# Performance work log

Measured on AMD Instinct MI355X. Metric: run time of the kernel, lower is better.

The kernel has to match this reference:

```python
import jax, jax.numpy as jnp
import numpy as np

NUM_HEADS = 16


def setup_inputs() -> dict:
    key = jax.random.key(0)
    ks = jax.random.split(key, 7)
    B, N, C, P = 8, 1024, 1024, 64
    H, hd = NUM_HEADS, C // NUM_HEADS
    return {
        "x": jax.random.normal(ks[0], (B, N, C), jnp.float32),
        "prompt": jax.random.normal(ks[1], (B, 2, P, H, hd), jnp.float32),
        "alpha": jax.random.uniform(ks[2], (1,), jnp.float32),
        "half_alpha": jax.random.uniform(ks[3], (1,), jnp.float32),
        "Wqkv": jax.random.normal(ks[4], (3 * C, C), jnp.float32) * 0.02,
        "Wproj": jax.random.normal(ks[5], (C, C), jnp.float32) * 0.02,
        "bproj": jnp.zeros((C,), jnp.float32),
    }


def reference(x, prompt, alpha, half_alpha, Wqkv, Wproj, bproj):
    B, N, C = x.shape
    H = NUM_HEADS
    hd = C // H
    scale = hd ** -0.5
    a = alpha[0]
    ha = half_alpha[0]
    # QKV projection (no bias): [B,N,3C] -> [3,B,H,N,hd]
    qkv = (x @ Wqkv.T).reshape(B, N, 3, H, hd).transpose(2, 0, 3, 1, 4)
    q, k, v = qkv[0], qkv[1], qkv[2]
    # prompt [B,2,P,H,hd] -> [2,B,H,P,hd]
    pr = prompt.transpose(1, 0, 3, 2, 4)
    key_prefix, value_prefix = pr[0], pr[1]
    # prefix concat with elementwise scaling
    k = jnp.concatenate([key_prefix, k * ha], axis=2) * a  # [B,H,P+N,hd]
    v = jnp.concatenate([value_prefix, v * ha], axis=2) * a
    attn = jax.nn.softmax(jnp.einsum('bhqd,bhkd->bhqk', q, k) * scale, axis=-1)
    out = jnp.einsum('bhqk,bhkd->bhqd', attn, v)  # [B,H,N,hd]
    out = out.transpose(0, 2, 1, 3).reshape(B, N, C)
    return out @ Wproj.T + bproj
```

## Files before the change

kernel.cpp:

```cpp
#include <hip/hip_runtime.h>

typedef float f32x4 __attribute__((ext_vector_type(4)));
typedef short bf16x8 __attribute__((ext_vector_type(8)));

#define NB 8
#define NH 16
#define NSEQ 1024
#define NP 64
#define NKV 1088
#define NC 1024
#define NHD 64
#define BHSZ 69632

__device__ __forceinline__ unsigned short f2bf(float f) {
  unsigned int u = __builtin_bit_cast(unsigned int, f);
  u += 0x7fffu + ((u >> 16) & 1u);
  return (unsigned short)(u >> 16);
}

__device__ __forceinline__ f32x4 mfma16(bf16x8 a, bf16x8 b, f32x4 c) {
  return __builtin_amdgcn_mfma_f32_16x16x32_bf16(a, b, c, 0, 0, 0);
}

__device__ __forceinline__ size_t fa_elem(int r, int k) {
  return (size_t)(r >> 7) * 131072 + (size_t)(k >> 6) * 8192 + ((r >> 6) & 1) * 4096 +
         ((k >> 5) & 1) * 2048 + ((r >> 4) & 3) * 512 + (((k >> 3) & 3) * 16 + (r & 15)) * 8 +
         (k & 7);
}

__device__ __forceinline__ void fragpack_chunk(const float* __restrict__ src,
                                               unsigned short* __restrict__ dst, int c) {
  const int lane = c & 63, m = (c >> 6) & 3, kk = (c >> 8) & 1, wr = (c >> 9) & 1,
            t = (c >> 10) & 15, panel = c >> 14;
  const int row = panel * 128 + wr * 64 + m * 16 + (lane & 15);
  const int k = t * 64 + kk * 32 + (lane >> 4) * 8;
  const float* s = src + (size_t)row * 1024 + k;
  const float4 v0 = *(const float4*)s;
  const float4 v1 = *(const float4*)(s + 4);
  ushort4 o0, o1;
  o0.x = f2bf(v0.x); o0.y = f2bf(v0.y); o0.z = f2bf(v0.z); o0.w = f2bf(v0.w);
  o1.x = f2bf(v1.x); o1.y = f2bf(v1.y); o1.z = f2bf(v1.z); o1.w = f2bf(v1.w);
  *(ushort4*)(dst + (size_t)c * 8) = o0;
  *(ushort4*)(dst + (size_t)c * 8 + 4) = o1;
}

__global__ void pack_fused(const float* __restrict__ x, const float* __restrict__ wq,
                           const float* __restrict__ wp, const float* __restrict__ prompt,
                           unsigned short* __restrict__ xd, unsigned short* __restrict__ wqd,
                           unsigned short* __restrict__ wpd, unsigned short* __restrict__ Kf,
                           unsigned short* __restrict__ Vf, const float* __restrict__ alpha) {
  int gid = blockIdx.x * 256 + threadIdx.x;
  if (gid < 1048576) {
    fragpack_chunk(x, xd, gid);
  } else if (gid < 1441792) {
    fragpack_chunk(wq, wqd, gid - 1048576);
  } else if (gid < 1572864) {
    fragpack_chunk(wp, wpd, gid - 1441792);
  } else {
    int i = gid - 1572864;
    float a = alpha[0];
    int d4 = i & 15, p = (i >> 4) & 63, h = (i >> 10) & 15, b = i >> 14;
    const int bh = b * 16 + h;
    const int d0 = d4 * 4;
    const float4 kv4 = *(const float4*)(prompt + ((((size_t)(b * 2 + 0) * NP + p) * NH + h) * NHD + d0));
    {
      const int mk = p >> 4, lrk = p & 15, kk = d0 >> 5, lg = (d0 >> 3) & 3, e0 = d0 & 7;
      unsigned short* kd = Kf + (size_t)bh * BHSZ + ((mk * 2 + kk) * 4 + lg) * 128 + lrk * 8 + e0;
      kd[0] = f2bf(kv4.x * a); kd[1] = f2bf(kv4.y * a);
      kd[2] = f2bf(kv4.z * a); kd[3] = f2bf(kv4.w * a);
    }
    const float4 vv4 = *(const float4*)(prompt + ((((size_t)(b * 2 + 1) * NP + p) * NH + h) * NHD + d0));
    {
      const int df = d0 >> 4, kk = p >> 5, lg = (p >> 3) & 3, e = p & 7;
      unsigned short* vd = Vf + (size_t)bh * BHSZ + ((df * 2 + kk) * 4 + lg) * 128 + e;
      vd[((d0 + 0) & 15) * 8] = f2bf(vv4.x * a);
      vd[((d0 + 1) & 15) * 8] = f2bf(vv4.y * a);
      vd[((d0 + 2) & 15) * 8] = f2bf(vv4.z * a);
      vd[((d0 + 3) & 15) * 8] = f2bf(vv4.w * a);
    }
  }
}

template <int MODE>
__global__ __launch_bounds__(256, 2)
void gemm_direct(const unsigned short* __restrict__ Af, const unsigned short* __restrict__ Bf,
                 unsigned short* __restrict__ Qg, unsigned short* __restrict__ Kf,
                 unsigned short* __restrict__ Vf,
                 const float* __restrict__ alphap, const float* __restrict__ halfp,
                 float* __restrict__ Cout, const float* __restrict__ bias) {
  const int tid = threadIdx.x, lane = tid & 63, wv = tid >> 6;
  const int wr = wv >> 1, wc = wv & 1;
  const int lg = lane >> 4, lr = lane & 15;
  const int bx = blockIdx.x, by = blockIdx.y;

  const unsigned short* Ab = Af + (size_t)bx * 131072 + wr * 4096 + lane * 8;
  const unsigned short* Bb = Bf + (size_t)by * 131072 + wc * 4096 + lane * 8;

  f32x4 acc[4][4] = {};
  bf16x8 aC[2][4], bC[2][4], aN[2][4], bN[2][4];

#define LOADA(dst, t)                                                          \
  _Pragma("unroll") for (int kk = 0; kk < 2; ++kk)                             \
  _Pragma("unroll") for (int m = 0; m < 4; ++m)                                \
      dst[kk][m] = *(const bf16x8*)(Ab + (size_t)(t) * 8192 + kk * 2048 + m * 512)
#define LOADB(dst, t)                                                          \
  _Pragma("unroll") for (int kk = 0; kk < 2; ++kk)                             \
  _Pragma("unroll") for (int n = 0; n < 4; ++n)                                \
      dst[kk][n] = *(const bf16x8*)(Bb + (size_t)(t) * 8192 + kk * 2048 + n * 512)

  LOADA(aC, 0);
  LOADB(bC, 0);
#pragma unroll
  for (int t = 0; t < 16; ++t) {
    if (t < 15) { LOADA(aN, t + 1); LOADB(bN, t + 1); }
    __builtin_amdgcn_sched_barrier(0);
    __builtin_amdgcn_s_setprio(1);
#pragma unroll
    for (int kk = 0; kk < 2; ++kk)
#pragma unroll
      for (int m = 0; m < 4; ++m)
#pragma unroll
        for (int n = 0; n < 4; ++n)
          acc[m][n] = mfma16(aC[kk][m], bC[kk][n], acc[m][n]);
    __builtin_amdgcn_s_setprio(0);
#pragma unroll
    for (int kk = 0; kk < 2; ++kk)
#pragma unroll
      for (int i = 0; i < 4; ++i) { aC[kk][i] = aN[kk][i]; bC[kk][i] = bN[kk][i]; }
  }
#undef LOADA
#undef LOADB

  if constexpr (MODE == 0) {
    const int slot = (by * 128) >> 10;
    const int csIn = (by * 128) & 1023;
    const float sc = (slot == 0) ? 0.18033688011112042f : (alphap[0] * halfp[0]);
#pragma unroll
    for (int m = 0; m < 4; ++m) {
      const int grow0 = bx * 128 + wr * 64 + m * 16 + lg * 4;
#pragma unroll
      for (int n = 0; n < 4; ++n) {
        const int gcol = csIn + wc * 64 + n * 16 + lr;
        const int h = gcol >> 6, d = gcol & 63;
#pragma unroll
        for (int j = 0; j < 4; ++j) {
          const int grow = grow0 + j;
          const int b = grow >> 10, nn = grow & 1023;
          const int bh = b * 16 + h;
          const unsigned short u = f2bf(acc[m][n][j] * sc);
          if (slot == 0) {
            Qg[((size_t)bh * NSEQ + nn) * NHD + d] = u;
          } else if (slot == 1) {
            const int kv = NP + nn;
            const int t = kv >> 6, mk = (kv >> 4) & 3, lrk = kv & 15;
            const int kkk = d >> 5, lgk = (d >> 3) & 3, e = d & 7;
            Kf[(size_t)bh * BHSZ + (size_t)((t * 4 + mk) * 2 + kkk) * 512 + (lgk * 16 + lrk) * 8 + e] = u;
          } else {
            const int kv = NP + nn;
            const int t = kv >> 6, kkv = (kv >> 5) & 1, lgv = (kv >> 3) & 3, e = kv & 7;
            const int df = d >> 4, lrv = d & 15;
            Vf[(size_t)bh * BHSZ + (size_t)((t * 4 + df) * 2 + kkv) * 512 + (lgv * 16 + lrv) * 8 + e] = u;
          }
        }
      }
    }
  } else {
#pragma unroll
    for (int m = 0; m < 4; ++m) {
      const int grow0 = bx * 128 + wr * 64 + m * 16 + lg * 4;
#pragma unroll
      for (int n = 0; n < 4; ++n) {
        const int gcol = by * 128 + wc * 64 + n * 16 + lr;
        const float bb = bias[gcol];
#pragma unroll
        for (int j = 0; j < 4; ++j)
          Cout[(size_t)(grow0 + j) * NC + gcol] = acc[m][n][j] + bb;
      }
    }
  }
}

__global__ __launch_bounds__(256, 3)
void attn_fwd(const unsigned short* __restrict__ Qg, const unsigned short* __restrict__ Kf,
              const unsigned short* __restrict__ Vf, unsigned short* __restrict__ Oat) {
  __shared__ __align__(16) unsigned short Plds[4 * 32 * 64];
  const int tid = threadIdx.x, lane = tid & 63, wv = tid >> 6;
  const int bh = blockIdx.x & 127;
  const int q0 = (blockIdx.x >> 7) * 128;
  const int lg = lane >> 4, lr = lane & 15;

  bf16x8 bq[2][2];
#pragma unroll
  for (int nq = 0; nq < 2; ++nq)
#pragma unroll
    for (int kk = 0; kk < 2; ++kk)
      bq[nq][kk] = *(const bf16x8*)(Qg + ((size_t)bh * NSEQ + q0 + wv * 32 + nq * 16 + lr) * NHD + kk * 32 + lg * 8);

  f32x4 oac[2][4] = {};
  float mrun[2] = {-1e30f, -1e30f};
  float lrun[2] = {0.f, 0.f};

  const unsigned short* Kb = Kf + (size_t)bh * BHSZ + lane * 8;
  const unsigned short* Vb = Vf + (size_t)bh * BHSZ + lane * 8;
  unsigned short* Pw = Plds + wv * 2048;

  for (int t = 0; t < 17; ++t) {
    bf16x8 ak[4][2];
#pragma unroll
    for (int mk = 0; mk < 4; ++mk)
#pragma unroll
      for (int kk = 0; kk < 2; ++kk)
        ak[mk][kk] = *(const bf16x8*)(Kb + (size_t)((t * 4 + mk) * 2 + kk) * 512);

    f32x4 sa[4][2] = {};
    __builtin_amdgcn_s_setprio(1);
#pragma unroll
    for (int kk = 0; kk < 2; ++kk)
#pragma unroll
      for (int mk = 0; mk < 4; ++mk)
#pragma unroll
        for (int nq = 0; nq < 2; ++nq)
          sa[mk][nq] = mfma16(ak[mk][kk], bq[nq][kk], sa[mk][nq]);
    __builtin_amdgcn_s_setprio(0);

    bf16x8 bv[4][2];
#pragma unroll
    for (int df = 0; df < 4; ++df)
#pragma unroll
      for (int kk = 0; kk < 2; ++kk)
        bv[df][kk] = *(const bf16x8*)(Vb + (size_t)((t * 4 + df) * 2 + kk) * 512);

    float tmx[2];
#pragma unroll
    for (int nq = 0; nq < 2; ++nq) {
      f32x4 m4 = sa[0][nq];
#pragma unroll
      for (int mk = 1; mk < 4; ++mk)
#pragma unroll
        for (int j = 0; j < 4; ++j) m4[j] = fmaxf(m4[j], sa[mk][nq][j]);
      float tm = fmaxf(fmaxf(m4[0], m4[1]), fmaxf(m4[2], m4[3]));
      tm = fmaxf(tm, __shfl_xor(tm, 16));
      tm = fmaxf(tm, __shfl_xor(tm, 32));
      tmx[nq] = tm;
    }
    const bool upd = !__all((tmx[0] <= mrun[0] + 8.f) && (tmx[1] <= mrun[1] + 8.f));
    if (upd) {
      const float nm0 = fmaxf(mrun[0], tmx[0]);
      const float nm1 = fmaxf(mrun[1], tmx[1]);
      const float e0 = __builtin_amdgcn_exp2f(mrun[0] - nm0);
      const float e1 = __builtin_amdgcn_exp2f(mrun[1] - nm1);
      mrun[0] = nm0; mrun[1] = nm1;
      lrun[0] *= e0; lrun[1] *= e1;
#pragma unroll
      for (int m = 0; m < 2; ++m)
#pragma unroll
        for (int j = 0; j < 4; ++j) {
          const float fe = __shfl(m ? e1 : e0, lg * 4 + j, 16);
#pragma unroll
          for (int df = 0; df < 4; ++df) oac[m][df][j] *= fe;
        }
    }
#pragma unroll
    for (int nq = 0; nq < 2; ++nq) {
#pragma unroll
      for (int mk = 0; mk < 4; ++mk)
#pragma unroll
        for (int j = 0; j < 4; ++j)
          sa[mk][nq][j] = __builtin_amdgcn_exp2f(sa[mk][nq][j] - mrun[nq]);
      f32x4 s4 = sa[0][nq];
#pragma unroll
      for (int mk = 1; mk < 4; ++mk)
#pragma unroll
        for (int j = 0; j < 4; ++j) s4[j] += sa[mk][nq][j];
      float s = (s4[0] + s4[1]) + (s4[2] + s4[3]);
      s += __shfl_xor(s, 16);
      s += __shfl_xor(s, 32);
      lrun[nq] += s;
      const int q = nq * 16 + lr;
#pragma unroll
      for (int mk = 0; mk < 4; ++mk) {
        const int c = mk * 2 + (lg >> 1);
        uint2 uu;
        uu.x = (unsigned)f2bf(sa[mk][nq][0]) | ((unsigned)f2bf(sa[mk][nq][1]) << 16);
        uu.y = (unsigned)f2bf(sa[mk][nq][2]) | ((unsigned)f2bf(sa[mk][nq][3]) << 16);
        *(uint2*)(Pw + q * 64 + ((c ^ (q & 7)) << 3) + (lg & 1) * 4) = uu;
      }
    }

    __builtin_amdgcn_s_setprio(1);
#pragma unroll
    for (int kk = 0; kk < 2; ++kk) {
      bf16x8 ap[2];
#pragma unroll
      for (int m = 0; m < 2; ++m) {
        const int q = m * 16 + lr;
        const int pos = (kk * 4 + lg) ^ (q & 7);
        ap[m] = *(const bf16x8*)(Pw + q * 64 + pos * 8);
      }
#pragma unroll
      for (int m = 0; m < 2; ++m)
#pragma unroll
        for (int df = 0; df < 4; ++df)
          oac[m][df] = mfma16(ap[m], bv[df][kk], oac[m][df]);
    }
    __builtin_amdgcn_s_setprio(0);
  }

  const int bidx = bh >> 4, h = bh & 15;
  const float l0 = 1.f / lrun[0], l1 = 1.f / lrun[1];
#pragma unroll
  for (int m = 0; m < 2; ++m) {
#pragma unroll
    for (int j = 0; j < 4; ++j) {
      const float fi = __shfl(m ? l1 : l0, lg * 4 + j, 16);
      const int grow = bidx * NSEQ + q0 + wv * 32 + m * 16 + lg * 4 + j;
#pragma unroll
      for (int df = 0; df < 4; ++df) {
        const int col = h * 64 + df * 16 + lr;
        Oat[fa_elem(grow, col)] = f2bf(oac[m][df][j] * fi);
      }
    }
  }
}

extern "C" void kernel_launch(void* const* d_in, const int* in_sizes, int n_in,
                              void* d_out, int out_size, void* d_ws, size_t ws_size,
                              hipStream_t stream) {
  const float* x      = (const float*)d_in[0];
  const float* prompt = (const float*)d_in[1];
  const float* alpha  = (const float*)d_in[2];
  const float* halfa  = (const float*)d_in[3];
  const float* Wqkv   = (const float*)d_in[4];
  const float* Wproj  = (const float*)d_in[5];
  const float* bproj  = (const float*)d_in[6];
  float* out = (float*)d_out;

  unsigned short* ws    = (unsigned short*)d_ws;
  unsigned short* x_bf  = ws;
  unsigned short* w_bf  = x_bf + (size_t)8192 * 1024;
  unsigned short* wp_bf = w_bf + (size_t)3072 * 1024;
  unsigned short* Qg    = wp_bf + (size_t)1024 * 1024;
  unsigned short* Kf    = Qg + (size_t)NB * NH * NSEQ * NHD;
  unsigned short* Vf    = Kf + (size_t)128 * BHSZ;
  unsigned short* Oat   = Vf + (size_t)128 * BHSZ;

  pack_fused<<<6656, 256, 0, stream>>>(x, Wqkv, Wproj, prompt, x_bf, w_bf, wp_bf,
                                       Kf, Vf, alpha);

  gemm_direct<0><<<dim3(64, 24), 256, 0, stream>>>(x_bf, w_bf, Qg, Kf, Vf, alpha, halfa,
                                                   nullptr, nullptr);
  attn_fwd<<<1024, 256, 0, stream>>>(Qg, Kf, Vf, Oat);
  gemm_direct<1><<<dim3(64, 8), 256, 0, stream>>>(Oat, wp_bf, nullptr, nullptr, nullptr,
                                                  nullptr, nullptr, out, bproj);
}
```

Measured before the change: 165.3 us.

## Use inline-asm global loads with explicit vmcnt waits for two-deep prefetch

Replaces compiler-generated register-prefetch loads in the direct GEMM main loop with inline-assembly global_load_dwordx4 using SGPR base plus VGPR offset and immediate offsets. Two k-tiles are kept in flight in even/odd register buffers, with manual s_waitcnt vmcnt(16) so the MFMAs on one tile overlap the loads of the next two. This removes the register copies between buffers and is meant to hide global memory latency better. It depends on the asm volatile loads being counted correctly against vmcnt and on the compiler not reordering around them, and the extra in-flight buffer raises register pressure under launch bounds (256,2).

```diff
diff --git a/kernel.cpp b/kernel.cpp
--- a/kernel.cpp
+++ b/kernel.cpp
@@ -93,43 +93,67 @@
   const int lg = lane >> 4, lr = lane & 15;
   const int bx = blockIdx.x, by = blockIdx.y;
 
-  const unsigned short* Ab = Af + (size_t)bx * 131072 + wr * 4096 + lane * 8;
-  const unsigned short* Bb = Bf + (size_t)by * 131072 + wc * 4096 + lane * 8;
+  unsigned int vA0 = (unsigned)(bx * 131072 + wr * 4096 + lane * 8) * 2;
+  unsigned int vA1 = vA0 + 4096;
+  unsigned int vB0 = (unsigned)(by * 131072 + wc * 4096 + lane * 8) * 2;
+  unsigned int vB1 = vB0 + 4096;
 
   f32x4 acc[4][4] = {};
-  bf16x8 aC[2][4], bC[2][4], aN[2][4], bN[2][4];
-
-#define LOADA(dst, t)                                                          \
-  _Pragma("unroll") for (int kk = 0; kk < 2; ++kk)                             \
-  _Pragma("unroll") for (int m = 0; m < 4; ++m)                                \
-      dst[kk][m] = *(const bf16x8*)(Ab + (size_t)(t) * 8192 + kk * 2048 + m * 512)
-#define LOADB(dst, t)                                                          \
-  _Pragma("unroll") for (int kk = 0; kk < 2; ++kk)                             \
-  _Pragma("unroll") for (int n = 0; n < 4; ++n)                                \
-      dst[kk][n] = *(const bf16x8*)(Bb + (size_t)(t) * 8192 + kk * 2048 + n * 512)
-
-  LOADA(aC, 0);
-  LOADB(bC, 0);
+  bf16x8 aE[2][4], bE[2][4], aO[2][4], bO[2][4];
+
+#define GLD(dst, voff, base, imm)                                              \
+  asm volatile("global_load_dwordx4 %0, %1, %2 offset:" #imm                   \
+               : "=v"(dst) : "v"(voff), "s"(base))
+
+#define ISSUE_T(aX, bX)                                                        \
+  do {                                                                         \
+    GLD(aX[0][0], vA0, Af, 0);                                                 \
+    GLD(aX[0][1], vA0, Af, 1024);                                              \
+    GLD(aX[0][2], vA0, Af, 2048);                                              \
+    GLD(aX[0][3], vA0, Af, 3072);                                              \
+    GLD(aX[1][0], vA1, Af, 0);                                                 \
+    GLD(aX[1][1], vA1, Af, 1024);                                              \
+    GLD(aX[1][2], vA1, Af, 2048);                                              \
+    GLD(aX[1][3], vA1, Af, 3072);                                              \
+    GLD(bX[0][0], vB0, Bf, 0);                                                 \
+    GLD(bX[0][1], vB0, Bf, 1024);                                              \
+    GLD(bX[0][2], vB0, Bf, 2048);                                              \
+    GLD(bX[0][3], vB0, Bf, 3072);                                              \
+    GLD(bX[1][0], vB1, Bf, 0);                                                 \
+    GLD(bX[1][1], vB1, Bf, 1024);                                              \
+    GLD(bX[1][2], vB1, Bf, 2048);                                              \
+    GLD(bX[1][3], vB1, Bf, 3072);                                              \
+    vA0 += 16384; vA1 += 16384; vB0 += 16384; vB1 += 16384;                    \
+  } while (0)
+
+#define MFMA_T(aX, bX)                                                         \
+  do {                                                                         \
+    __builtin_amdgcn_s_setprio(1);                                             \
+    _Pragma("unroll") for (int kk = 0; kk < 2; ++kk)                           \
+    _Pragma("unroll") for (int m = 0; m < 4; ++m)                              \
+    _Pragma("unroll") for (int n = 0; n < 4; ++n)                              \
+        acc[m][n] = mfma16(aX[kk][m], bX[kk][n], acc[m][n]);                   \
+    __builtin_amdgcn_s_setprio(0);                                             \
+  } while (0)
+
+  ISSUE_T(aE, bE);
+  ISSUE_T(aO, bO);
 #pragma unroll
   for (int t = 0; t < 16; ++t) {
-    if (t < 15) { LOADA(aN, t + 1); LOADB(bN, t + 1); }
+    if (t < 15) asm volatile("s_waitcnt vmcnt(16)" ::: "memory");
+    else        asm volatile("s_waitcnt vmcnt(0)" ::: "memory");
     __builtin_amdgcn_sched_barrier(0);
-    __builtin_amdgcn_s_setprio(1);
-#pragma unroll
-    for (int kk = 0; kk < 2; ++kk)
-#pragma unroll
-      for (int m = 0; m < 4; ++m)
-#pragma unroll
-        for (int n = 0; n < 4; ++n)
-          acc[m][n] = mfma16(aC[kk][m], bC[kk][n], acc[m][n]);
-    __builtin_amdgcn_s_setprio(0);
-#pragma unroll
-    for (int kk = 0; kk < 2; ++kk)
-#pragma unroll
-      for (int i = 0; i < 4; ++i) { aC[kk][i] = aN[kk][i]; bC[kk][i] = bN[kk][i]; }
-  }
-#undef LOADA
-#undef LOADB
+    if ((t & 1) == 0) {
+      MFMA_T(aE, bE);
+      if (t + 2 < 16) ISSUE_T(aE, bE);
+    } else {
+      MFMA_T(aO, bO);
+      if (t + 2 < 16) ISSUE_T(aO, bO);
+    }
+  }
+#undef GLD
+#undef ISSUE_T
+#undef MFMA_T
 
   if constexpr (MODE == 0) {
     const int slot = (by * 128) >> 10;
```

Result: no change. 165.5 us (+0.1%).

## Split GEMM tiles across eight waves with half-tile double buffering

Applied to the files above, without the earlier changes.

The direct-from-global GEMM now runs 512 threads per block, each wave owning a 64x32 sub-tile instead of 64x64. This halves per-wave accumulator and fragment registers. The k-loop is restructured into 32 half-steps with two alternating register buffers, so loads for step s+2 are issued right after the MFMAs of step s. The aim is higher occupancy and better latency hiding, at the cost of each wave reloading its A fragments, which doubles A global/L2 traffic per block.

```diff
diff --git a/kernel.cpp b/kernel.cpp
--- a/kernel.cpp
+++ b/kernel.cpp
@@ -82,54 +82,55 @@
 }
 
 template <int MODE>
-__global__ __launch_bounds__(256, 2)
+__global__ __launch_bounds__(512, 4)
 void gemm_direct(const unsigned short* __restrict__ Af, const unsigned short* __restrict__ Bf,
                  unsigned short* __restrict__ Qg, unsigned short* __restrict__ Kf,
                  unsigned short* __restrict__ Vf,
                  const float* __restrict__ alphap, const float* __restrict__ halfp,
                  float* __restrict__ Cout, const float* __restrict__ bias) {
   const int tid = threadIdx.x, lane = tid & 63, wv = tid >> 6;
-  const int wr = wv >> 1, wc = wv & 1;
+  const int wm = wv >> 2, wn = wv & 3;
   const int lg = lane >> 4, lr = lane & 15;
   const int bx = blockIdx.x, by = blockIdx.y;
 
-  const unsigned short* Ab = Af + (size_t)bx * 131072 + wr * 4096 + lane * 8;
-  const unsigned short* Bb = Bf + (size_t)by * 131072 + wc * 4096 + lane * 8;
-
-  f32x4 acc[4][4] = {};
-  bf16x8 aC[2][4], bC[2][4], aN[2][4], bN[2][4];
-
-#define LOADA(dst, t)                                                          \
-  _Pragma("unroll") for (int kk = 0; kk < 2; ++kk)                             \
-  _Pragma("unroll") for (int m = 0; m < 4; ++m)                                \
-      dst[kk][m] = *(const bf16x8*)(Ab + (size_t)(t) * 8192 + kk * 2048 + m * 512)
-#define LOADB(dst, t)                                                          \
-  _Pragma("unroll") for (int kk = 0; kk < 2; ++kk)                             \
-  _Pragma("unroll") for (int n = 0; n < 4; ++n)                                \
-      dst[kk][n] = *(const bf16x8*)(Bb + (size_t)(t) * 8192 + kk * 2048 + n * 512)
-
-  LOADA(aC, 0);
-  LOADB(bC, 0);
-#pragma unroll
-  for (int t = 0; t < 16; ++t) {
-    if (t < 15) { LOADA(aN, t + 1); LOADB(bN, t + 1); }
-    __builtin_amdgcn_sched_barrier(0);
-    __builtin_amdgcn_s_setprio(1);
-#pragma unroll
-    for (int kk = 0; kk < 2; ++kk)
-#pragma unroll
-      for (int m = 0; m < 4; ++m)
-#pragma unroll
-        for (int n = 0; n < 4; ++n)
-          acc[m][n] = mfma16(aC[kk][m], bC[kk][n], acc[m][n]);
-    __builtin_amdgcn_s_setprio(0);
-#pragma unroll
-    for (int kk = 0; kk < 2; ++kk)
-#pragma unroll
-      for (int i = 0; i < 4; ++i) { aC[kk][i] = aN[kk][i]; bC[kk][i] = bN[kk][i]; }
-  }
-#undef LOADA
-#undef LOADB
+  const unsigned short* Abase = Af + (size_t)bx * 131072 + wm * 4096 + lane * 8;
+  const unsigned short* Bbase = Bf + (size_t)by * 131072 + (wn >> 1) * 4096 + (wn & 1) * 1024 + lane * 8;
+
+  f32x4 acc[4][2] = {};
+  bf16x8 xa[4], xb[2], ya[4], yb[2];
+
+#define ISSUE(pa, pb, t, kk)                                                   \
+  do {                                                                         \
+    _Pragma("unroll") for (int m = 0; m < 4; ++m)                              \
+        pa[m] = *(const bf16x8*)(Abase + (size_t)(t) * 8192 + (kk) * 2048 + m * 512); \
+    _Pragma("unroll") for (int n = 0; n < 2; ++n)                              \
+        pb[n] = *(const bf16x8*)(Bbase + (size_t)(t) * 8192 + (kk) * 2048 + n * 512); \
+  } while (0)
+
+#define MM(pa, pb)                                                             \
+  do {                                                                         \
+    __builtin_amdgcn_s_setprio(1);                                             \
+    _Pragma("unroll") for (int m = 0; m < 4; ++m)                              \
+    _Pragma("unroll") for (int n = 0; n < 2; ++n)                              \
+        acc[m][n] = mfma16(pa[m], pb[n], acc[m][n]);                           \
+    __builtin_amdgcn_s_setprio(0);                                             \
+  } while (0)
+
+  ISSUE(xa, xb, 0, 0);
+  ISSUE(ya, yb, 0, 1);
+#pragma unroll
+  for (int s = 0; s < 32; ++s) {
+    const int t2 = (s + 2) >> 1, k2 = (s + 2) & 1;
+    if ((s & 1) == 0) {
+      MM(xa, xb);
+      if (s + 2 < 32) ISSUE(xa, xb, t2, k2);
+    } else {
+      MM(ya, yb);
+      if (s + 2 < 32) ISSUE(ya, yb, t2, k2);
+    }
+  }
+#undef ISSUE
+#undef MM
 
   if constexpr (MODE == 0) {
     const int slot = (by * 128) >> 10;
@@ -137,10 +138,10 @@
     const float sc = (slot == 0) ? 0.18033688011112042f : (alphap[0] * halfp[0]);
 #pragma unroll
     for (int m = 0; m < 4; ++m) {
-      const int grow0 = bx * 128 + wr * 64 + m * 16 + lg * 4;
-#pragma unroll
-      for (int n = 0; n < 4; ++n) {
-        const int gcol = csIn + wc * 64 + n * 16 + lr;
+      const int grow0 = bx * 128 + wm * 64 + m * 16 + lg * 4;
+#pragma unroll
+      for (int n = 0; n < 2; ++n) {
+        const int gcol = csIn + wn * 32 + n * 16 + lr;
         const int h = gcol >> 6, d = gcol & 63;
 #pragma unroll
         for (int j = 0; j < 4; ++j) {
@@ -167,10 +168,10 @@
   } else {
 #pragma unroll
     for (int m = 0; m < 4; ++m) {
-      const int grow0 = bx * 128 + wr * 64 + m * 16 + lg * 4;
-#pragma unroll
-      for (int n = 0; n < 4; ++n) {
-        const int gcol = by * 128 + wc * 64 + n * 16 + lr;
+      const int grow0 = bx * 128 + wm * 64 + m * 16 + lg * 4;
+#pragma unroll
+      for (int n = 0; n < 2; ++n) {
+        const int gcol = by * 128 + wn * 32 + n * 16 + lr;
         const float bb = bias[gcol];
 #pragma unroll
         for (int j = 0; j < 4; ++j)
@@ -347,9 +348,9 @@
   pack_fused<<<6656, 256, 0, stream>>>(x, Wqkv, Wproj, prompt, x_bf, w_bf, wp_bf,
                                        Kf, Vf, alpha);
 
-  gemm_direct<0><<<dim3(64, 24), 256, 0, stream>>>(x_bf, w_bf, Qg, Kf, Vf, alpha, halfa,
+  gemm_direct<0><<<dim3(64, 24), 512, 0, stream>>>(x_bf, w_bf, Qg, Kf, Vf, alpha, halfa,
                                                    nullptr, nullptr);
   attn_fwd<<<1024, 256, 0, stream>>>(Qg, Kf, Vf, Oat);
-  gemm_direct<1><<<dim3(64, 8), 256, 0, stream>>>(Oat, wp_bf, nullptr, nullptr, nullptr,
+  gemm_direct<1><<<dim3(64, 8), 512, 0, stream>>>(Oat, wp_bf, nullptr, nullptr, nullptr,
                                                   nullptr, nullptr, out, bproj);
 }
```

Result: slower. 190.9 us (+15.4%).

## Use wider 256x128 tiles with half-step double buffering in QKV GEMM

Applied to the files above, without the earlier changes.

Splits the templated GEMM into a dedicated QKV kernel and a projection kernel. The QKV kernel now has each block compute a 256x128 tile, with every wave owning 64 full rows times 128 columns. It pipelines loads at half-k-step granularity using two alternating register buffers. The aim is more MFMA work per B-operand load and better overlap of global loads with MFMA, at the cost of more accumulator registers. The projection GEMM also drops its sched_barrier, which lets the compiler interleave loads with MFMAs.

```diff
diff --git a/kernel.cpp b/kernel.cpp
--- a/kernel.cpp
+++ b/kernel.cpp
@@ -81,13 +81,92 @@
   }
 }
 
-template <int MODE>
 __global__ __launch_bounds__(256, 2)
-void gemm_direct(const unsigned short* __restrict__ Af, const unsigned short* __restrict__ Bf,
-                 unsigned short* __restrict__ Qg, unsigned short* __restrict__ Kf,
-                 unsigned short* __restrict__ Vf,
-                 const float* __restrict__ alphap, const float* __restrict__ halfp,
-                 float* __restrict__ Cout, const float* __restrict__ bias) {
+void gemm_qkv_w(const unsigned short* __restrict__ Af, const unsigned short* __restrict__ Bf,
+                unsigned short* __restrict__ Qg, unsigned short* __restrict__ Kf,
+                unsigned short* __restrict__ Vf,
+                const float* __restrict__ alphap, const float* __restrict__ halfp) {
+  const int tid = threadIdx.x, lane = tid & 63, wv = tid >> 6;
+  const int lg = lane >> 4, lr = lane & 15;
+  const int bx = blockIdx.x, by = blockIdx.y;
+
+  const unsigned short* Abase = Af + (size_t)(bx * 2 + (wv >> 1)) * 131072 + (wv & 1) * 4096 + lane * 8;
+  const unsigned short* Bbase = Bf + (size_t)by * 131072 + lane * 8;
+
+  f32x4 acc[4][8] = {};
+  bf16x8 xa[4], xb[8], ya[4], yb[8];
+
+#define ISSUE(pa, pb, t, kk)                                                       \
+  do {                                                                             \
+    _Pragma("unroll") for (int m = 0; m < 4; ++m)                                  \
+        pa[m] = *(const bf16x8*)(Abase + (size_t)(t) * 8192 + (kk) * 2048 + m * 512); \
+    _Pragma("unroll") for (int n = 0; n < 8; ++n)                                  \
+        pb[n] = *(const bf16x8*)(Bbase + (size_t)(t) * 8192 + (kk) * 2048 +        \
+                                 (n >> 2) * 4096 + (n & 3) * 512);                 \
+  } while (0)
+
+#define MM(pa, pb)                                                                 \
+  do {                                                                             \
+    __builtin_amdgcn_s_setprio(1);                                                 \
+    _Pragma("unroll") for (int m = 0; m < 4; ++m)                                  \
+    _Pragma("unroll") for (int n = 0; n < 8; ++n)                                  \
+        acc[m][n] = mfma16(pa[m], pb[n], acc[m][n]);                               \
+    __builtin_amdgcn_s_setprio(0);                                                 \
+  } while (0)
+
+  ISSUE(xa, xb, 0, 0);
+  ISSUE(ya, yb, 0, 1);
+#pragma unroll
+  for (int s = 0; s < 32; ++s) {
+    const int t2 = (s + 2) >> 1, k2 = (s + 2) & 1;
+    if ((s & 1) == 0) {
+      MM(xa, xb);
+      if (s + 2 < 32) ISSUE(xa, xb, t2, k2);
+    } else {
+      MM(ya, yb);
+      if (s + 2 < 32) ISSUE(ya, yb, t2, k2);
+    }
+  }
+#undef ISSUE
+#undef MM
+
+  const int slot = by >> 3;
+  const int csIn = (by & 7) * 128;
+  const float sc = (slot == 0) ? 0.18033688011112042f : (alphap[0] * halfp[0]);
+#pragma unroll
+  for (int m = 0; m < 4; ++m) {
+    const int grow0 = bx * 256 + wv * 64 + m * 16 + lg * 4;
+#pragma unroll
+    for (int n = 0; n < 8; ++n) {
+      const int gcol = csIn + n * 16 + lr;
+      const int h = gcol >> 6, d = gcol & 63;
+#pragma unroll
+      for (int j = 0; j < 4; ++j) {
+        const int grow = grow0 + j;
+        const int b = grow >> 10, nn = grow & 1023;
+        const int bh = b * 16 + h;
+        const unsigned short u = f2bf(acc[m][n][j] * sc);
+        if (slot == 0) {
+          Qg[((size_t)bh * NSEQ + nn) * NHD + d] = u;
+        } else if (slot == 1) {
+          const int kv = NP + nn;
+          const int t = kv >> 6, mk = (kv >> 4) & 3, lrk = kv & 15;
+          const int kkk = d >> 5, lgk = (d >> 3) & 3, e = d & 7;
+          Kf[(size_t)bh * BHSZ + (size_t)((t * 4 + mk) * 2 + kkk) * 512 + (lgk * 16 + lrk) * 8 + e] = u;
+        } else {
+          const int kv = NP + nn;
+          const int t = kv >> 6, kkv = (kv >> 5) & 1, lgv = (kv >> 3) & 3, e = kv & 7;
+          const int df = d >> 4, lrv = d & 15;
+          Vf[(size_t)bh * BHSZ + (size_t)((t * 4 + df) * 2 + kkv) * 512 + (lgv * 16 + lrv) * 8 + e] = u;
+        }
+      }
+    }
+  }
+}
+
+__global__ __launch_bounds__(256, 2)
+void gemm_proj(const unsigned short* __restrict__ Af, const unsigned short* __restrict__ Bf,
+               float* __restrict__ Cout, const float* __restrict__ bias) {
   const int tid = threadIdx.x, lane = tid & 63, wv = tid >> 6;
   const int wr = wv >> 1, wc = wv & 1;
   const int lg = lane >> 4, lr = lane & 15;
@@ -113,7 +192,6 @@
 #pragma unroll
   for (int t = 0; t < 16; ++t) {
     if (t < 15) { LOADA(aN, t + 1); LOADB(bN, t + 1); }
-    __builtin_amdgcn_sched_barrier(0);
     __builtin_amdgcn_s_setprio(1);
 #pragma unroll
     for (int kk = 0; kk < 2; ++kk)
@@ -131,51 +209,16 @@
 #undef LOADA
 #undef LOADB
 
-  if constexpr (MODE == 0) {
-    const int slot = (by * 128) >> 10;
-    const int csIn = (by * 128) & 1023;
-    const float sc = (slot == 0) ? 0.18033688011112042f : (alphap[0] * halfp[0]);
-#pragma unroll
-    for (int m = 0; m < 4; ++m) {
-      const int grow0 = bx * 128 + wr * 64 + m * 16 + lg * 4;
-#pragma unroll
-      for (int n = 0; n < 4; ++n) {
-        const int gcol = csIn + wc * 64 + n * 16 + lr;
-        const int h = gcol >> 6, d = gcol & 63;
-#pragma unroll
-        for (int j = 0; j < 4; ++j) {
-          const int grow = grow0 + j;
-          const int b = grow >> 10, nn = grow & 1023;
-          const int bh = b * 16 + h;
-          const unsigned short u = f2bf(acc[m][n][j] * sc);
-          if (slot == 0) {
-            Qg[((size_t)bh * NSEQ + nn) * NHD + d] = u;
-          } else if (slot == 1) {
-            const int kv = NP + nn;
-            const int t = kv >> 6, mk = (kv >> 4) & 3, lrk = kv & 15;
-            const int kkk = d >> 5, lgk = (d >> 3) & 3, e = d & 7;
-            Kf[(size_t)bh * BHSZ + (size_t)((t * 4 + mk) * 2 + kkk) * 512 + (lgk * 16 + lrk) * 8 + e] = u;
-          } else {
-            const int kv = NP + nn;
-            const int t = kv >> 6, kkv = (kv >> 5) & 1, lgv = (kv >> 3) & 3, e = kv & 7;
-            const int df = d >> 4, lrv = d & 15;
-            Vf[(size_t)bh * BHSZ + (size_t)((t * 4 + df) * 2 + kkv) * 512 + (lgv * 16 + lrv) * 8 + e] = u;
-          }
-        }
-      }
-    }
-  } else {
-#pragma unroll
-    for (int m = 0; m < 4; ++m) {
-      const int grow0 = bx * 128 + wr * 64 + m * 16 + lg * 4;
-#pragma unroll
-      for (int n = 0; n < 4; ++n) {
-        const int gcol = by * 128 + wc * 64 + n * 16 + lr;
-        const float bb = bias[gcol];
-#pragma unroll
-        for (int j = 0; j < 4; ++j)
-          Cout[(size_t)(grow0 + j) * NC + gcol] = acc[m][n][j] + bb;
-      }
+#pragma unroll
+  for (int m = 0; m < 4; ++m) {
+    const int grow0 = bx * 128 + wr * 64 + m * 16 + lg * 4;
+#pragma unroll
+    for (int n = 0; n < 4; ++n) {
+      const int gcol = by * 128 + wc * 64 + n * 16 + lr;
+      const float bb = bias[gcol];
+#pragma unroll
+      for (int j = 0; j < 4; ++j)
+        Cout[(size_t)(grow0 + j) * NC + gcol] = acc[m][n][j] + bb;
     }
   }
 }
@@ -347,9 +390,7 @@
   pack_fused<<<6656, 256, 0, stream>>>(x, Wqkv, Wproj, prompt, x_bf, w_bf, wp_bf,
                                        Kf, Vf, alpha);
 
-  gemm_direct<0><<<dim3(64, 24), 256, 0, stream>>>(x_bf, w_bf, Qg, Kf, Vf, alpha, halfa,
-                                                   nullptr, nullptr);
+  gemm_qkv_w<<<dim3(32, 24), 256, 0, stream>>>(x_bf, w_bf, Qg, Kf, Vf, alpha, halfa);
   attn_fwd<<<1024, 256, 0, stream>>>(Qg, Kf, Vf, Oat);
-  gemm_direct<1><<<dim3(64, 8), 256, 0, stream>>>(Oat, wp_bf, nullptr, nullptr, nullptr,
-                                                  nullptr, nullptr, out, bproj);
-}
+  gemm_proj<<<dim3(64, 8), 256, 0, stream>>>(Oat, wp_bf, out, bproj);
+}
```

Result: faster. 157.8 us (-4.6%).
